# Kernel optimization log

Measured on AMD Instinct MI355X. Metric: run time of the kernel, lower is better.

The kernel has to match this reference:

```python
import jax, jax.numpy as jnp
import numpy as np
from jax import lax

DIM = 128
HEADS = 2
SR = 4
HID = 512  # 4 * DIM
DROPKEY_P = 0.1


def _ln(x, g, b, eps=1e-5):
    m = jnp.mean(x, axis=-1, keepdims=True)
    v = jnp.var(x, axis=-1, keepdims=True)
    return (x - m) / jnp.sqrt(v + eps) * g + b


def _block(x, H, W, params, key):
    (n1g, n1b, qw, kvw, srw, srb, sng, snb, pw, pb,
     n2g, n2b, f1w, f1b, dww, dwb, f2w, f2b) = params
    B, N, C = x.shape
    dh = C // HEADS
    scale = dh ** -0.5
    # --- spatial-reduction attention ---
    h = _ln(x, n1g, n1b)
    q = (h @ qw.T).reshape(B, N, HEADS, dh).transpose(0, 2, 1, 3)  # [B,h,N,dh]
    xi = h.transpose(0, 2, 1).reshape(B, C, H, W)
    xs = lax.conv_general_dilated(xi, srw, (SR, SR), 'VALID',
                                  dimension_numbers=('NCHW', 'OIHW', 'NCHW'))
    xs = xs + srb[None, :, None, None]
    Np = (H // SR) * (W // SR)
    xs = xs.reshape(B, C, Np).transpose(0, 2, 1)  # [B,N',C]
    xs = _ln(xs, sng, snb)
    kv = (xs @ kvw.T).reshape(B, Np, 2, HEADS, dh).transpose(2, 0, 3, 1, 4)
    k, v = kv[0], kv[1]  # [B,h,N',dh]
    attn = jnp.einsum('bhnd,bhmd->bhnm', q, k) * scale
    # dropkey: bernoulli(p) mask pushed to -1e12 before softmax (always applied)
    mask = jax.random.bernoulli(key, DROPKEY_P, attn.shape)
    attn = attn + mask.astype(attn.dtype) * (-1e12)
    attn = jax.nn.softmax(attn, axis=-1)
    o = jnp.einsum('bhnm,bhmd->bhnd', attn, v).transpose(0, 2, 1, 3).reshape(B, N, C)
    x = x + o @ pw.T + pb
    # --- MLP with depthwise conv ---
    h2 = _ln(x, n2g, n2b)
    h2 = h2 @ f1w.T + f1b  # [B,N,HID]
    hi = h2.transpose(0, 2, 1).reshape(B, HID, H, W)
    hi = lax.conv_general_dilated(hi, dww, (1, 1), 'SAME',
                                  feature_group_count=HID,
                                  dimension_numbers=('NCHW', 'OIHW', 'NCHW'))
    hi = hi + dwb[None, :, None, None]
    h2 = hi.reshape(B, HID, N).transpose(0, 2, 1)
    h2 = jax.nn.gelu(h2, approximate=False)
    x = x + h2 @ f2w.T + f2b
    return x


def setup_inputs() -> dict:
    key = jax.random.key(0)
    ks = jax.random.split(key, 10)
    p = {}
    p['x'] = jax.random.normal(ks[0], (16, 2 * DIM, 56, 56), jnp.float32)
    p['concat_w'] = jax.random.normal(ks[1], (DIM, 2 * DIM), jnp.float32) * 0.02
    p['concat_b'] = jnp.zeros((DIM,), jnp.float32)
    # two Blocks -> leading dim 2 on all per-block params
    p['norm1_g'] = jnp.ones((2, DIM), jnp.float32)
    p['norm1_b'] = jnp.zeros((2, DIM), jnp.float32)
    p['q_w'] = jax.random.normal(ks[2], (2, DIM, DIM), jnp.float32) * 0.02
    p['kv_w'] = jax.random.normal(ks[3], (2, 2 * DIM, DIM), jnp.float32) * 0.02
    p['sr_w'] = jax.random.normal(ks[4], (2, DIM, DIM, SR, SR), jnp.float32) * 0.03
    p['sr_b'] = jnp.zeros((2, DIM), jnp.float32)
    p['srn_g'] = jnp.ones((2, DIM), jnp.float32)
    p['srn_b'] = jnp.zeros((2, DIM), jnp.float32)
    p['proj_w'] = jax.random.normal(ks[5], (2, DIM, DIM), jnp.float32) * 0.02
    p['proj_b'] = jnp.zeros((2, DIM), jnp.float32)
    p['norm2_g'] = jnp.ones((2, DIM), jnp.float32)
    p['norm2_b'] = jnp.zeros((2, DIM), jnp.float32)
    p['fc1_w'] = jax.random.normal(ks[6], (2, HID, DIM), jnp.float32) * 0.02
    p['fc1_b'] = jnp.zeros((2, HID), jnp.float32)
    p['dw_w'] = jax.random.normal(ks[7], (2, HID, 1, 3, 3), jnp.float32) * 0.1
    p['dw_b'] = jnp.zeros((2, HID), jnp.float32)
    p['fc2_w'] = jax.random.normal(ks[8], (2, DIM, HID), jnp.float32) * 0.02
    p['fc2_b'] = jnp.zeros((2, DIM), jnp.float32)
    return p


def reference(x, concat_w, concat_b, norm1_g, norm1_b, q_w, kv_w, sr_w, sr_b,
              srn_g, srn_b, proj_w, proj_b, norm2_g, norm2_b, fc1_w, fc1_b,
              dw_w, dw_b, fc2_w, fc2_b):
    b, c, h, w = x.shape
    xs = x.transpose(0, 2, 3, 1).reshape(b, h * w, c)
    xs = xs @ concat_w.T + concat_b  # [B,N,DIM]
    mkey = jax.random.key(42)
    stacked = (norm1_g, norm1_b, q_w, kv_w, sr_w, sr_b, srn_g, srn_b, proj_w,
               proj_b, norm2_g, norm2_b, fc1_w, fc1_b, dw_w, dw_b, fc2_w, fc2_b)
    for i in range(2):
        params_i = tuple(p[i] for p in stacked)
        xs = _block(xs, h, w, params_i, jax.random.fold_in(mkey, i))
    return xs.reshape(b, h, w, DIM).transpose(0, 3, 1, 2)
```

## Files before the change

kernel.cpp:

```cpp
#include <hip/hip_runtime.h>
#include <stdint.h>

typedef __attribute__((ext_vector_type(8))) short short8;
typedef __attribute__((ext_vector_type(4))) float f32x4;
typedef __attribute__((ext_vector_type(2))) float f32x2;
typedef unsigned short u16;
typedef uint32_t u32;
typedef unsigned long long u64;

__host__ __device__ static inline void threefry(u32 k0, u32 k1, u32 x0, u32 x1,
                                                u32* o0, u32* o1) {
  u32 ks2 = k0 ^ k1 ^ 0x1BD11BDAu;
  x0 += k0; x1 += k1;
#define TF_RR(r) { x0 += x1; x1 = (x1 << (r)) | (x1 >> (32 - (r))); x1 ^= x0; }
  TF_RR(13) TF_RR(15) TF_RR(26) TF_RR(6)
  x0 += k1;  x1 += ks2 + 1u;
  TF_RR(17) TF_RR(29) TF_RR(16) TF_RR(24)
  x0 += ks2; x1 += k0 + 2u;
  TF_RR(13) TF_RR(15) TF_RR(26) TF_RR(6)
  x0 += k0;  x1 += k1 + 3u;
  TF_RR(17) TF_RR(29) TF_RR(16) TF_RR(24)
  x0 += k1;  x1 += ks2 + 4u;
  TF_RR(13) TF_RR(15) TF_RR(26) TF_RR(6)
  x0 += ks2; x1 += k0 + 5u;
#undef TF_RR
  *o0 = x0; *o1 = x1;
}

__device__ static inline float bf2f(u16 u) {
  union { u32 i; float f; } v; v.i = ((u32)u) << 16; return v.f;
}
__device__ static inline u16 f2bf(float f) {
  union { float f; u32 i; } v; v.f = f;
  u32 x = v.i;
  return (u16)((x + 0x7FFFu + ((x >> 16) & 1u)) >> 16);
}
__device__ static inline float lo_bf(u32 w) {
  union { u32 i; float f; } v; v.i = w << 16; return v.f;
}
__device__ static inline float hi_bf(u32 w) {
  union { u32 i; float f; } v; v.i = w & 0xFFFF0000u; return v.f;
}
__device__ static inline bool is_f32(const u32* ng) { return ng[0] == 0x3F800000u; }

typedef const uint32_t __attribute__((address_space(1)))* gas_ptr;
typedef uint32_t __attribute__((address_space(3)))* las_ptr;
__device__ static inline void gld16(const u16* g, u16* l) {
  __builtin_amdgcn_global_load_lds((gas_ptr)(const void*)g, (las_ptr)(void*)l, 16, 0, 0);
}

#define MASK_HALF 9834496u
#define MASK_HALFWORDS 307328

__global__ __launch_bounds__(256) void mask_gen(u32* __restrict__ Mw, u32 k0, u32 k1) {
  int w = blockIdx.x * 256 + threadIdx.x;
  if (w >= MASK_HALFWORDS) return;
  u32 bits0 = 0, bits1 = 0;
  u32 base = (u32)w * 32u;
  for (int i = 0; i < 32; i++) {
    u32 o0, o1;
    threefry(k0, k1, base + (u32)i, base + (u32)i + MASK_HALF, &o0, &o1);
    union { u32 u; float f; } u0, u1;
    u0.u = (o0 >> 9) | 0x3F800000u;
    u1.u = (o1 >> 9) | 0x3F800000u;
    if (u0.f - 1.0f < 0.1f) bits0 |= (1u << i);
    if (u1.f - 1.0f < 0.1f) bits1 |= (1u << i);
  }
  Mw[w] = bits0;
  Mw[w + MASK_HALFWORDS] = bits1;
}

__global__ __launch_bounds__(256) void mask_repack(const u32* __restrict__ MSK,
                                                   u32* __restrict__ MSK2) {
  int t = blockIdx.x * 256 + threadIdx.x;
  if (t >= 702464) return;
  int row = t / 7, w = t - row * 7;
  u32 f0 = (u32)row * 196u + (u32)w * 32u;
  u32 lo = MSK[f0 >> 5], hi = MSK[(f0 >> 5) + 1];
  int sh = f0 & 31;
  MSK2[t] = sh ? ((lo >> sh) | (hi << (32 - sh))) : lo;
}

__global__ __launch_bounds__(256) void zero_vt(u32* __restrict__ VT) {
  int t = blockIdx.x * 256 + threadIdx.x;
  if (t < 229376) VT[t] = 0;
}

struct PtrTab { const void* p[20]; };
#define ARENA_N 963968

__global__ __launch_bounds__(256) void convert_params(PtrTab tab, u16* __restrict__ arena) {
  const int cum[21] = {0, 32768, 32896, 33152, 33408, 66176, 131712, 656000, 656256,
                       656512, 656768, 689536, 689792, 690048, 690304, 821376, 822400,
                       831616, 832640, 963712, 963968};
  int idx = blockIdx.x * 256 + threadIdx.x;
  if (idx >= ARENA_N) return;
  bool f32m = (((const u32*)tab.p[2])[0] == 0x3F800000u);
  int t = 0;
  while (idx >= cum[t + 1]) t++;
  int local = idx - cum[t];
  if (t == 16) {
    int blk = local / 4608, r = local - blk * 4608;
    int wi = r >> 9, c = r & 511;
    local = blk * 4608 + c * 9 + wi;
  }
  u16 v;
  if (f32m) v = f2bf(((const float*)tab.p[t])[local]);
  else      v = ((const u16*)tab.p[t])[local];
  arena[idx] = v;
}

__global__ __launch_bounds__(256) void transpose_in(const void* __restrict__ Xin,
                                                    const u32* __restrict__ ng,
                                                    u16* __restrict__ Xt) {
  bool f32m = is_f32(ng);
  __shared__ u16 tile[64][65];
  int n0 = blockIdx.x * 64, c0 = blockIdx.y * 64, b = blockIdx.z;
  int tx = threadIdx.x & 63, ty = threadIdx.x >> 6;
  if (f32m) {
    const float* src = (const float*)Xin + (size_t)b * 256 * 3136;
#pragma unroll
    for (int i = 0; i < 16; i++) {
      int cl = i * 4 + ty;
      tile[cl][tx] = f2bf(src[(size_t)(c0 + cl) * 3136 + n0 + tx]);
    }
  } else {
    const u16* src = (const u16*)Xin + (size_t)b * 256 * 3136;
#pragma unroll
    for (int i = 0; i < 16; i++) {
      int cl = i * 4 + ty;
      tile[cl][tx] = src[(size_t)(c0 + cl) * 3136 + n0 + tx];
    }
  }
  __syncthreads();
  u16* dst = Xt + (size_t)b * 3136 * 256;
#pragma unroll
  for (int i = 0; i < 16; i++) {
    int nl = i * 4 + ty;
    dst[(size_t)(n0 + nl) * 256 + c0 + tx] = tile[tx][nl];
  }
}

__global__ __launch_bounds__(256) void transpose_out(const float* __restrict__ X,
                                                     const u32* __restrict__ ng,
                                                     void* __restrict__ Out) {
  bool f32m = is_f32(ng);
  __shared__ float tile[64][65];
  int n0 = blockIdx.x * 64, d0 = blockIdx.y * 64, b = blockIdx.z;
  int tx = threadIdx.x & 63, ty = threadIdx.x >> 6;
#pragma unroll
  for (int i = 0; i < 16; i++) {
    int nl = i * 4 + ty;
    tile[nl][tx] = X[((size_t)b * 3136 + n0 + nl) * 128 + d0 + tx];
  }
  __syncthreads();
#pragma unroll
  for (int i = 0; i < 16; i++) {
    int dl = i * 4 + ty;
    size_t o = ((size_t)b * 128 + d0 + dl) * 3136 + n0 + tx;
    if (f32m) ((float*)Out)[o] = tile[tx][dl];
    else      ((u16*)Out)[o]   = f2bf(tile[tx][dl]);
  }
}

__global__ __launch_bounds__(256) void ln_kernel(const float* __restrict__ X,
                                                 const u16* __restrict__ G,
                                                 const u16* __restrict__ Bi,
                                                 u16* __restrict__ Out, int rows) {
  int row = blockIdx.x * 4 + (threadIdx.x >> 6);
  if (row >= rows) return;
  int lane = threadIdx.x & 63;
  const float* xp = X + (size_t)row * 128;
  float a = xp[lane], c = xp[lane + 64];
  float s1 = a + c, s2 = a * a + c * c;
#pragma unroll
  for (int d = 1; d < 64; d <<= 1) {
    s1 += __shfl_xor(s1, d);
    s2 += __shfl_xor(s2, d);
  }
  float mean = s1 * 0.0078125f;
  float var = s2 * 0.0078125f - mean * mean;
  float inv = 1.0f / sqrtf(var + 1e-5f);
  Out[(size_t)row * 128 + lane] = f2bf((a - mean) * inv * bf2f(G[lane]) + bf2f(Bi[lane]));
  Out[(size_t)row * 128 + lane + 64] =
      f2bf((c - mean) * inv * bf2f(G[lane + 64]) + bf2f(Bi[lane + 64]));
}

__global__ __launch_bounds__(256) void im2col_sr(const u16* __restrict__ H,
                                                 u16* __restrict__ Acol) {
  int t = blockIdx.x * 256 + threadIdx.x;
  int c = t & 127;
  int rest = t >> 7;
  int ij = rest & 15;
  int row = rest >> 4;
  int i = ij >> 2, j = ij & 3;
  int bb = row / 196, pp = row - bb * 196;
  int ph = pp / 14, pw = pp - ph * 14;
  int n = (4 * ph + i) * 56 + 4 * pw + j;
  Acol[(size_t)row * 2048 + c * 16 + ij] = H[((size_t)bb * 3136 + n) * 128 + c];
}

__global__ __launch_bounds__(256) __attribute__((amdgpu_waves_per_eu(2, 4)))
void gemm_tiled(const u16* __restrict__ A,
                const u16* __restrict__ W,
                const u16* __restrict__ bias,
                float* __restrict__ outF,
                u16* __restrict__ outB,
                u16* __restrict__ outVT,
                int M, int N, int K, int mode) {
  __shared__ __align__(16) u16 smem[16896];
  u16* AlsP = smem;
  u16* BlsP = smem + 8192;
  int n0 = blockIdx.x * 128, m0 = blockIdx.y * 128;
  int tid = threadIdx.x, wv = tid >> 6, lane = tid & 63;
  int wr = wv >> 1, wc = wv & 1;
  int l15 = lane & 15, hh = lane >> 4, lk = hh * 8;
  int srow = wv * 32 + (lane >> 2);
  int scol = (lane & 3) * 8;

  f32x4 acc[4][4];
#pragma unroll
  for (int m = 0; m < 4; m++)
#pragma unroll
    for (int n = 0; n < 4; n++) acc[m][n] = (f32x4){0.f, 0.f, 0.f, 0.f};

#define STAGE(buf, k0)                                                          \
  {                                                                             \
    _Pragma("unroll") for (int i = 0; i < 2; i++) {                             \
      int ar = m0 + srow + i * 16;                                              \
      if (ar >= M) ar = M - 1;                                                  \
      gld16(A + (size_t)ar * K + (k0) + scol,                                   \
            AlsP + (buf) * 4096 + (wv * 32 + i * 16) * 32);                     \
      int br = n0 + srow + i * 16;                                              \
      gld16(W + (size_t)br * K + (k0) + scol,                                   \
            BlsP + (buf) * 4096 + (wv * 32 + i * 16) * 32);                     \
    }                                                                           \
  }

  int nt = K >> 5;
  STAGE(0, 0);
  int cur = 0;
  for (int t = 0; t < nt; t++) {
    __syncthreads();
    if (t + 1 < nt) STAGE(cur ^ 1, (t + 1) * 32);
    short8 af[4], bf[4];
#pragma unroll
    for (int m = 0; m < 4; m++)
      af[m] = *(const short8*)(AlsP + cur * 4096 + (wr * 64 + m * 16 + l15) * 32 + lk);
#pragma unroll
    for (int n = 0; n < 4; n++)
      bf[n] = *(const short8*)(BlsP + cur * 4096 + (wc * 64 + n * 16 + l15) * 32 + lk);
#pragma unroll
    for (int m = 0; m < 4; m++)
#pragma unroll
      for (int n = 0; n < 4; n++)
        acc[m][n] = __builtin_amdgcn_mfma_f32_16x16x32_bf16(af[m], bf[n], acc[m][n], 0, 0, 0);
    cur ^= 1;
  }
#undef STAGE

  if (mode == 0) {
    __syncthreads();
#pragma unroll
    for (int n = 0; n < 4; n++) {
      int col = wc * 64 + n * 16 + l15;
      float bv = bias ? bf2f(bias[n0 + col]) : 0.0f;
#pragma unroll
      for (int m = 0; m < 4; m++) {
        int rbase = wr * 64 + m * 16 + hh * 4;
#pragma unroll
        for (int r = 0; r < 4; r++)
          smem[(rbase + r) * 132 + col] = f2bf(acc[m][n][r] + bv);
      }
    }
    __syncthreads();
#pragma unroll
    for (int p = 0; p < 8; p++) {
      int row = p * 16 + (tid >> 4);
      int colb = (tid & 15) * 8;
      int grow = m0 + row;
      if (grow < M) {
        short8 v = *(const short8*)&smem[row * 132 + colb];
        *(short8*)(outB + (size_t)grow * N + n0 + colb) = v;
      }
    }
    return;
  }

#pragma unroll
  for (int n = 0; n < 4; n++) {
    int col = n0 + wc * 64 + n * 16 + l15;
    float bv = bias ? bf2f(bias[col]) : 0.0f;
#pragma unroll
    for (int m = 0; m < 4; m++) {
      int rbase = m0 + wr * 64 + m * 16 + hh * 4;
#pragma unroll
      for (int r = 0; r < 4; r++) {
        int row = rbase + r;
        if (row < M) {
          float v = acc[m][n][r] + bv;
          if (mode == 1) outF[(size_t)row * N + col] = v;
          else if (mode == 2) outF[(size_t)row * N + col] += v;
          else {
            if (col < 128) outB[(size_t)row * 128 + col] = f2bf(v);
            else {
              int hd = (col - 128) >> 6, d = (col - 128) & 63;
              int b = row / 196, key = row - b * 196;
              outVT[(size_t)((b * 2 + hd) * 64 + d) * 224 + key] = f2bf(v);
            }
          }
        }
      }
    }
  }
}

__global__ __launch_bounds__(256) __attribute__((amdgpu_waves_per_eu(2, 4)))
void gemm_n128(const u16* __restrict__ A,
               const u16* __restrict__ W,
               const u16* __restrict__ bias,
               float* __restrict__ outF,
               u16* __restrict__ outB,
               const u16* __restrict__ lnG,
               const u16* __restrict__ lnB,
               u16* __restrict__ outH,
               int M, int K, int mode) {
  __shared__ __align__(16) u16 smem[12288];
  __shared__ float sumsA[64][4];
  __shared__ float sumsB[64][4];
  u16* Als = smem;
  u16* Bls = smem + 4096;
  int m0 = blockIdx.y * 64;
  int tid = threadIdx.x, wv = tid >> 6, lane = tid & 63;
  int l15 = lane & 15, hq = lane >> 4, lk = hq * 8;
  int scol = (lane & 3) * 8;

  f32x4 acc[4][2];
#pragma unroll
  for (int m = 0; m < 4; m++)
#pragma unroll
    for (int n = 0; n < 2; n++) acc[m][n] = (f32x4){0.f, 0.f, 0.f, 0.f};

#define STAGE(buf, k0)                                                          \
  {                                                                             \
    int ar = m0 + wv * 16 + (lane >> 2);                                        \
    if (ar >= M) ar = M - 1;                                                    \
    gld16(A + (size_t)ar * K + (k0) + scol, Als + (buf) * 2048 + wv * 512);     \
    _Pragma("unroll") for (int i = 0; i < 2; i++) {                             \
      int br = wv * 32 + i * 16 + (lane >> 2);                                  \
      gld16(W + (size_t)br * K + (k0) + scol,                                   \
            Bls + (buf) * 4096 + wv * 1024 + i * 512);                          \
    }                                                                           \
  }

  int nt = K >> 5;
  STAGE(0, 0);
  int cur = 0;
  for (int t = 0; t < nt; t++) {
    __syncthreads();
    if (t + 1 < nt) STAGE(cur ^ 1, (t + 1) * 32);
    short8 af[4], bf[2];
#pragma unroll
    for (int m = 0; m < 4; m++)
      af[m] = *(const short8*)(Als + cur * 2048 + (m * 16 + l15) * 32 + lk);
#pragma unroll
    for (int n = 0; n < 2; n++)
      bf[n] = *(const short8*)(Bls + cur * 4096 + (wv * 32 + n * 16 + l15) * 32 + lk);
#pragma unroll
    for (int m = 0; m < 4; m++)
#pragma unroll
      for (int n = 0; n < 2; n++)
        acc[m][n] = __builtin_amdgcn_mfma_f32_16x16x32_bf16(af[m], bf[n], acc[m][n], 0, 0, 0);
    cur ^= 1;
  }
#undef STAGE

  if (mode == 2) {
#pragma unroll
    for (int n = 0; n < 2; n++) {
      int col = wv * 32 + n * 16 + l15;
      float bv = bias ? bf2f(bias[col]) : 0.0f;
#pragma unroll
      for (int m = 0; m < 4; m++) {
        int rbase = m0 + m * 16 + hq * 4;
#pragma unroll
        for (int r = 0; r < 4; r++)
          outF[(size_t)(rbase + r) * 128 + col] += acc[m][n][r] + bv;
      }
    }
    return;
  }

  if (mode >= 4) {
#pragma unroll
    for (int n = 0; n < 2; n++) {
      int col = wv * 32 + n * 16 + l15;
      float bv = bias ? bf2f(bias[col]) : 0.0f;
#pragma unroll
      for (int m = 0; m < 4; m++) {
        int rbase = m0 + m * 16 + hq * 4;
#pragma unroll
        for (int r = 0; r < 4; r++) {
          float v = acc[m][n][r] + bv;
          if (mode == 5) v += outF[(size_t)(rbase + r) * 128 + col];
          acc[m][n][r] = v;
          outF[(size_t)(rbase + r) * 128 + col] = v;
        }
      }
    }
#pragma unroll
    for (int m = 0; m < 4; m++) {
#pragma unroll
      for (int r = 0; r < 4; r++) {
        float a = acc[m][0][r] + acc[m][1][r];
        float b = acc[m][0][r] * acc[m][0][r] + acc[m][1][r] * acc[m][1][r];
#pragma unroll
        for (int d = 1; d < 16; d <<= 1) {
          a += __shfl_xor(a, d);
          b += __shfl_xor(b, d);
        }
        if (l15 == 0) {
          int lrow = m * 16 + hq * 4 + r;
          sumsA[lrow][wv] = a;
          sumsB[lrow][wv] = b;
        }
      }
    }
    __syncthreads();
#pragma unroll
    for (int m = 0; m < 4; m++) {
#pragma unroll
      for (int r = 0; r < 4; r++) {
        int lrow = m * 16 + hq * 4 + r;
        float t1 = sumsA[lrow][0] + sumsA[lrow][1] + sumsA[lrow][2] + sumsA[lrow][3];
        float t2 = sumsB[lrow][0] + sumsB[lrow][1] + sumsB[lrow][2] + sumsB[lrow][3];
        float mean = t1 * 0.0078125f;
        float var = t2 * 0.0078125f - mean * mean;
        float inv = 1.0f / sqrtf(var + 1e-5f);
#pragma unroll
        for (int n = 0; n < 2; n++) {
          int col = wv * 32 + n * 16 + l15;
          float g = bf2f(lnG[col]), bb2 = bf2f(lnB[col]);
          smem[lrow * 132 + col] = f2bf((acc[m][n][r] - mean) * inv * g + bb2);
        }
      }
    }
    __syncthreads();
#pragma unroll
    for (int p = 0; p < 4; p++) {
      int row = p * 16 + (tid >> 4);
      int colb = (tid & 15) * 8;
      short8 v = *(const short8*)&smem[row * 132 + colb];
      *(short8*)(outH + (size_t)(m0 + row) * 128 + colb) = v;
    }
    return;
  }

  __syncthreads();
#pragma unroll
  for (int n = 0; n < 2; n++) {
    int col = wv * 32 + n * 16 + l15;
    float bv = bias ? bf2f(bias[col]) : 0.0f;
#pragma unroll
    for (int m = 0; m < 4; m++) {
      int rbase = m * 16 + hq * 4;
#pragma unroll
      for (int r = 0; r < 4; r++)
        smem[(rbase + r) * 132 + col] = f2bf(acc[m][n][r] + bv);
    }
  }
  __syncthreads();
#pragma unroll
  for (int p = 0; p < 4; p++) {
    int row = p * 16 + (tid >> 4);
    int colb = (tid & 15) * 8;
    short8 v = *(const short8*)&smem[row * 132 + colb];
    *(short8*)(outB + (size_t)(m0 + row) * 128 + colb) = v;
  }
}

__global__ __launch_bounds__(256) void gemm_splitk(const u16* __restrict__ A,
                                                   const u16* __restrict__ W,
                                                   float* __restrict__ PS,
                                                   int M, int N, int K) {
  __shared__ __align__(16) u16 Als[2][4096];
  __shared__ __align__(16) u16 Bls[2][4096];
  int n0 = blockIdx.x * 128, m0 = blockIdx.y * 128, ks = blockIdx.z;
  int tid = threadIdx.x, wv = tid >> 6, lane = tid & 63;
  int wr = wv >> 1, wc = wv & 1;
  int l15 = lane & 15, lk = (lane >> 4) * 8;
  int srow = wv * 32 + (lane >> 2);
  int scol = (lane & 3) * 8;

  f32x4 acc[4][4];
#pragma unroll
  for (int m = 0; m < 4; m++)
#pragma unroll
    for (int n = 0; n < 4; n++) acc[m][n] = (f32x4){0.f, 0.f, 0.f, 0.f};

#define STAGE(buf, k0)                                                          \
  {                                                                             \
    _Pragma("unroll") for (int i = 0; i < 2; i++) {                             \
      int ar = m0 + srow + i * 16;                                              \
      if (ar >= M) ar = M - 1;                                                  \
      gld16(A + (size_t)ar * K + (k0) + scol,                                   \
            &Als[buf][(wv * 32 + i * 16) * 32]);                                \
      int br = n0 + srow + i * 16;                                              \
      gld16(W + (size_t)br * K + (k0) + scol,                                   \
            &Bls[buf][(wv * 32 + i * 16) * 32]);                                \
    }                                                                           \
  }

  int kbeg = ks * 128;
  STAGE(0, kbeg);
  int cur = 0;
  for (int t = 0; t < 4; t++) {
    __syncthreads();
    if (t + 1 < 4) STAGE(cur ^ 1, kbeg + (t + 1) * 32);
    short8 af[4], bf[4];
#pragma unroll
    for (int m = 0; m < 4; m++)
      af[m] = *(const short8*)(&Als[cur][(wr * 64 + m * 16 + l15) * 32 + lk]);
#pragma unroll
    for (int n = 0; n < 4; n++)
      bf[n] = *(const short8*)(&Bls[cur][(wc * 64 + n * 16 + l15) * 32 + lk]);
#pragma unroll
    for (int m = 0; m < 4; m++)
#pragma unroll
      for (int n = 0; n < 4; n++)
        acc[m][n] = __builtin_amdgcn_mfma_f32_16x16x32_bf16(af[m], bf[n], acc[m][n], 0, 0, 0);
    cur ^= 1;
  }
#undef STAGE

  float* myPS = PS + (size_t)ks * M * N;
#pragma unroll
  for (int n = 0; n < 4; n++) {
    int col = n0 + wc * 64 + n * 16 + l15;
#pragma unroll
    for (int m = 0; m < 4; m++) {
      int rbase = m0 + wr * 64 + m * 16 + (lane >> 4) * 4;
#pragma unroll
      for (int r = 0; r < 4; r++) {
        int row = rbase + r;
        if (row < M) myPS[(size_t)row * N + col] = acc[m][n][r];
      }
    }
  }
}

__global__ __launch_bounds__(256) void splitk_reduce(const float* __restrict__ PS,
                                                     const u16* __restrict__ bias,
                                                     float* __restrict__ XS) {
  int t = blockIdx.x * 256 + threadIdx.x;
  if (t >= 401408) return;
  float s = bf2f(bias[t & 127]);
#pragma unroll
  for (int k = 0; k < 16; k++) s += PS[(size_t)k * 401408 + t];
  XS[t] = s;
}

__global__ __launch_bounds__(256) __attribute__((amdgpu_waves_per_eu(2, 4)))
void attn_kernel(const u16* __restrict__ Q,
                 const u16* __restrict__ Kb,
                 const u16* __restrict__ VT,
                 const u32* __restrict__ M2,
                 u16* __restrict__ O) {
  __shared__ __align__(16) u16 smA[14848];
  int t = blockIdx.x;
  int tp = (t & 7) * 196 + (t >> 3);
  int bh = tp / 49, qt = tp - bh * 49;
  int b = bh >> 1, hd = bh & 1;
  int q0 = qt * 64;
  int tid = threadIdx.x;

  int wv = tid >> 6, lane = tid & 63;
  int l15 = lane & 15, h = lane >> 4, lk = h * 8;

  {
    const u16* ksrc = Kb + (size_t)b * 196 * 128 + hd * 64;
    for (int idx = tid; idx < 1568; idx += 256) {
      int row = idx >> 3, ch = idx & 7;
      short8 v = *(const short8*)(ksrc + (size_t)row * 128 + ch * 8);
      *(short8*)&smA[row * 68 + ch * 8] = v;
    }
  }

  const u16* qp = Q + ((size_t)(b * 3136 + q0 + wv * 16 + l15) * 128) + hd * 64 + lk;
  short8 aq0 = *(const short8*)(qp);
  short8 aq1 = *(const short8*)(qp + 32);
  int rowg = q0 + wv * 16 + h * 4;

  u32 mwv[4][7];
  const u32* mwbase = M2 + (size_t)(bh * 3136 + rowg) * 7;
#pragma unroll
  for (int r = 0; r < 4; r++)
#pragma unroll
    for (int w = 0; w < 7; w++) mwv[r][w] = mwbase[r * 7 + w];

  __syncthreads();

  float sarr[13][4];
#pragma unroll
  for (int cc = 0; cc < 13; cc++) {
    int key = cc * 16 + l15;
    int keyc = key > 195 ? 195 : key;
    short8 kb0 = *(const short8*)&smA[keyc * 68 + lk];
    short8 kb1 = *(const short8*)&smA[keyc * 68 + 32 + lk];
    f32x4 s = {0.f, 0.f, 0.f, 0.f};
    s = __builtin_amdgcn_mfma_f32_16x16x32_bf16(aq0, kb0, s, 0, 0, 0);
    s = __builtin_amdgcn_mfma_f32_16x16x32_bf16(aq1, kb1, s, 0, 0, 0);
#pragma unroll
    for (int r = 0; r < 4; r++) sarr[cc][r] = s[r] * 0.125f;
  }

#pragma unroll
  for (int cc = 0; cc < 13; cc++) {
    bool keyok = (cc * 16 + l15) < 196;
    int pos = (cc & 3) * 16 + l15;
#pragma unroll
    for (int r = 0; r < 4; r++) {
      u64 mm = (cc < 4) ? ((u64)mwv[r][0] | ((u64)mwv[r][1] << 32))
             : (cc < 8) ? ((u64)mwv[r][2] | ((u64)mwv[r][3] << 32))
             : (cc < 12) ? ((u64)mwv[r][4] | ((u64)mwv[r][5] << 32))
                         : ((u64)mwv[r][6]);
      bool drop = (mm >> pos) & 1ull;
      if (!keyok || drop) sarr[cc][r] = -3.0e38f;
    }
  }

  float mx[4] = {sarr[0][0], sarr[0][1], sarr[0][2], sarr[0][3]};
#pragma unroll
  for (int cc = 1; cc < 13; cc++)
#pragma unroll
    for (int r = 0; r < 4; r++) mx[r] = fmaxf(mx[r], sarr[cc][r]);
#pragma unroll
  for (int d = 1; d < 16; d <<= 1)
#pragma unroll
    for (int r = 0; r < 4; r++) mx[r] = fmaxf(mx[r], __shfl_xor(mx[r], d));
  float sm[4] = {0.f, 0.f, 0.f, 0.f};
#pragma unroll
  for (int cc = 0; cc < 13; cc++)
#pragma unroll
    for (int r = 0; r < 4; r++) {
      float p = __expf(sarr[cc][r] - mx[r]);
      sarr[cc][r] = p;
      sm[r] += p;
    }
#pragma unroll
  for (int d = 1; d < 16; d <<= 1)
#pragma unroll
    for (int r = 0; r < 4; r++) sm[r] += __shfl_xor(sm[r], d);
  float inv[4];
#pragma unroll
  for (int r = 0; r < 4; r++)
    asm("v_rcp_f32 %0, %1" : "=v"(inv[r]) : "v"(sm[r]));

  __syncthreads();

#pragma unroll
  for (int cc = 0; cc < 13; cc++)
#pragma unroll
    for (int r = 0; r < 4; r++)
      smA[(wv * 16 + h * 4 + r) * 232 + cc * 16 + l15] = f2bf(sarr[cc][r] * inv[r]);
#pragma unroll
  for (int rj = 0; rj < 4; rj++) smA[(wv * 16 + l15) * 232 + 208 + h * 4 + rj] = 0;

  const u16* vbase = VT + (size_t)(bh * 64) * 224;
  short8 vw[4];
#pragma unroll
  for (int i = 0; i < 4; i++) {
    vw[i] = *(const short8*)(vbase + (size_t)(0 * 16 + l15) * 224 + i * 32 + lk);
  }
#pragma unroll
  for (int dc = 0; dc < 4; dc++) {
    f32x4 oa = {0.f, 0.f, 0.f, 0.f};
#pragma unroll
    for (int kc = 0; kc < 7; kc++) {
      int i = dc * 7 + kc;
      short8 bv = vw[i & 3];
      if (i + 4 < 28) {
        int i2 = i + 4;
        int dc2 = i2 / 7, kc2 = i2 - dc2 * 7;
        vw[i & 3] =
            *(const short8*)(vbase + (size_t)(dc2 * 16 + l15) * 224 + kc2 * 32 + lk);
      }
      short8 a = *(const short8*)&smA[(wv * 16 + l15) * 232 + kc * 32 + lk];
      oa = __builtin_amdgcn_mfma_f32_16x16x32_bf16(a, bv, oa, 0, 0, 0);
    }
#pragma unroll
    for (int r = 0; r < 4; r++) {
      O[((size_t)(b * 3136 + rowg + r) * 128) + hd * 64 + dc * 16 + l15] = f2bf(oa[r]);
    }
  }
}

__global__ __launch_bounds__(256) __attribute__((amdgpu_waves_per_eu(2, 4)))
void dwconv_gelu(const u16* __restrict__ H2,
                 const u16* __restrict__ Wdw,
                 const u16* __restrict__ Bdw,
                 u16* __restrict__ Out) {
  int tid = threadIdx.x;
  int wv = tid >> 6, lane = tid & 63;
  int sb = blockIdx.x;
  int wg = (sb & 7) * 392 + (sb >> 3);
  int strip = wg * 4 + wv;
  int bb = strip / 784;
  int s = strip - bb * 784;
  int y = s / 14, x0 = (s - y * 14) * 4;
  int c0 = lane * 8;

  f32x2 wf[9][4];
#pragma unroll
  for (int t9 = 0; t9 < 9; t9++) {
    short8 w8 = *(const short8*)(Wdw + t9 * 512 + c0);
#pragma unroll
    for (int p = 0; p < 4; p++) {
      u32 w = ((const u32*)&w8)[p];
      wf[t9][p] = (f32x2){lo_bf(w), hi_bf(w)};
    }
  }
  f32x2 acc[4][4];
  {
    short8 b8 = *(const short8*)(Bdw + c0);
#pragma unroll
    for (int p = 0; p < 4; p++) {
      u32 w = ((const u32*)&b8)[p];
      f32x2 bv = {lo_bf(w), hi_bf(w)};
#pragma unroll
      for (int q = 0; q < 4; q++) acc[q][p] = bv;
    }
  }

  const u16* base = H2 + ((size_t)bb * 3136) * 512 + c0;
#pragma unroll
  for (int di = -1; di <= 1; di++) {
    int y2 = y + di;
    if (y2 < 0 || y2 >= 56) continue;
    const u16* rowp = base + (size_t)(y2 * 56) * 512;
#pragma unroll
    for (int j = 0; j < 6; j++) {
      int c = x0 - 1 + j;
      if (c < 0 || c > 55) continue;
      short8 h8 = *(const short8*)(rowp + (size_t)c * 512);
      f32x2 hf[4];
#pragma unroll
      for (int p = 0; p < 4; p++) {
        u32 w = ((const u32*)&h8)[p];
        hf[p] = (f32x2){lo_bf(w), hi_bf(w)};
      }
      int wrow = (di + 1) * 3;
#pragma unroll
      for (int q = 0; q < 4; q++) {
        int dx = j - 1 - q;
        if (dx < -1 || dx > 1) continue;
#pragma unroll
        for (int p = 0; p < 4; p++) acc[q][p] += hf[p] * wf[wrow + dx + 1][p];
      }
    }
  }

  size_t obase = ((size_t)(bb * 3136 + y * 56 + x0)) * 512 + c0;
#pragma unroll
  for (int q = 0; q < 4; q++) {
    short8 ov;
#pragma unroll
    for (int p = 0; p < 4; p++) {
      float g2[2];
#pragma unroll
      for (int e = 0; e < 2; e++) {
        float v = acc[q][p][e];
        float tt = v * v;
        float yn = v * (-2.3022088f - 0.1029434f * tt);
        float ex;
        asm("v_exp_f32 %0, %1" : "=v"(ex) : "v"(yn));
        float den = 1.0f + ex;
        float sg;
        asm("v_rcp_f32 %0, %1" : "=v"(sg) : "v"(den));
        g2[e] = v * sg;
      }
      u32 pk;
      asm("v_cvt_pk_bf16_f32 %0, %1, %2" : "=v"(pk) : "v"(g2[0]), "v"(g2[1]));
      ((u32*)&ov)[p] = pk;
    }
    *(short8*)(Out + obase + (size_t)q * 512) = ov;
  }
}

__global__ __launch_bounds__(256) void fill_sentinel(void* __restrict__ Out,
                                                     const u32* __restrict__ ng, int n) {
  bool f32m = is_f32(ng);
  int t = blockIdx.x * 256 + threadIdx.x;
  if (t >= n) return;
  if (f32m) ((float*)Out)[t] = 12345.0f;
  else      ((u16*)Out)[t]   = f2bf(12345.0f);
}

extern "C" void kernel_launch(void* const* d_in, const int* in_sizes, int n_in,
                              void* d_out, int out_size, void* d_ws, size_t ws_size,
                              hipStream_t stream) {
  (void)in_sizes; (void)n_in;
  const u32* ng = (const u32*)d_in[3];

  const size_t o_X   = 0;
  const size_t o_H   = 25690112;
  const size_t o_R   = o_H + 12845056;
  const size_t o_Q   = o_R;
  const size_t o_O   = o_R + 12845056;
  const size_t o_Xt  = o_R + 25690112;
  const size_t o_H2C = o_R;
  const size_t o_H2  = o_R + 51380224;
  const size_t o_XS  = o_H2 + 51380224;
  const size_t o_XSN = o_XS + 1605632;
  const size_t o_KB  = o_XSN + 802816;
  const size_t o_VT  = o_KB + 802816;
  const size_t o_M2  = o_VT + 917504;
  const size_t o_AR  = o_M2 + 2809856;
  const size_t NEED  = o_AR + (size_t)ARENA_N * 2;

  if (ws_size < NEED) {
    fill_sentinel<<<(out_size + 255) / 256, 256, 0, stream>>>(d_out, ng, out_size);
    return;
  }

  char* ws = (char*)d_ws;
  float* X  = (float*)(ws + o_X);
  u16* H    = (u16*)(ws + o_H);
  u16* Qb   = (u16*)(ws + o_Q);
  u16* Ob   = (u16*)(ws + o_O);
  u16* Xt   = (u16*)(ws + o_Xt);
  u16* H2C  = (u16*)(ws + o_H2C);
  u16* H2   = (u16*)(ws + o_H2);
  float* PS = (float*)(ws + o_H2);
  float* XS = (float*)(ws + o_XS);
  u16* XSN  = (u16*)(ws + o_XSN);
  u16* Kb   = (u16*)(ws + o_KB);
  u16* VT   = (u16*)(ws + o_VT);
  u32* MSK  = (u32*)(ws + o_Xt);
  u32* MSK2 = (u32*)(ws + o_M2);
  u16* AR   = (u16*)(ws + o_AR);

  PtrTab tab;
  for (int j = 0; j < 20; j++) tab.p[j] = d_in[j + 1];
  convert_params<<<(ARENA_N + 255) / 256, 256, 0, stream>>>(tab, AR);
  zero_vt<<<896, 256, 0, stream>>>((u32*)VT);

  u16* ACW  = AR + 0;      u16* ACB  = AR + 32768;
  u16* AN1G = AR + 32896;  u16* AN1B = AR + 33152;
  u16* AQW  = AR + 33408;  u16* AKVW = AR + 66176;
  u16* ASRW = AR + 131712; u16* ASRB = AR + 656000;
  u16* ASNG = AR + 656256; u16* ASNB = AR + 656512;
  u16* APW  = AR + 656768; u16* APB  = AR + 689536;
  u16* AN2G = AR + 689792; u16* AN2B = AR + 690048;
  u16* AF1W = AR + 690304; u16* AF1B = AR + 821376;
  u16* ADWW = AR + 822400; u16* ADWB = AR + 831616;
  u16* AF2W = AR + 832640; u16* AF2B = AR + 963712;

  transpose_in<<<dim3(49, 4, 16), 256, 0, stream>>>(d_in[0], ng, Xt);
  gemm_n128<<<dim3(1, 784), 256, 0, stream>>>(Xt, ACW, ACB, X, nullptr,
                                              AN1G, AN1B, H, 50176, 256, 4);

  for (int i = 0; i < 2; i++) {
    u32 fk0, fk1;
    threefry(0u, 42u, 0u, (u32)i, &fk0, &fk1);

    gemm_n128<<<dim3(1, 784), 256, 0, stream>>>(H, AQW + i * 16384, nullptr, nullptr,
                                                Qb, nullptr, nullptr, nullptr,
                                                50176, 128, 0);
    im2col_sr<<<25088, 256, 0, stream>>>(H, Xt);
    gemm_splitk<<<dim3(1, 25, 16), 256, 0, stream>>>(Xt, ASRW + i * 262144, PS,
                                                     3136, 128, 2048);
    splitk_reduce<<<1568, 256, 0, stream>>>(PS, ASRB + i * 128, XS);
    mask_gen<<<1201, 256, 0, stream>>>(MSK, fk0, fk1);
    mask_repack<<<2744, 256, 0, stream>>>(MSK, MSK2);

    ln_kernel<<<784, 256, 0, stream>>>(XS, ASNG + i * 128, ASNB + i * 128, XSN, 3136);
    gemm_tiled<<<dim3(2, 25), 256, 0, stream>>>(XSN, AKVW + i * 32768, nullptr, nullptr,
                                                Kb, VT, 3136, 256, 128, 3);
    attn_kernel<<<1568, 256, 0, stream>>>(Qb, Kb, VT, MSK2, Ob);
    gemm_n128<<<dim3(1, 784), 256, 0, stream>>>(Ob, APW + i * 16384, APB + i * 128,
                                                X, nullptr,
                                                AN2G + i * 128, AN2B + i * 128, H,
                                                50176, 128, 5);
    gemm_tiled<<<dim3(4, 392), 256, 0, stream>>>(H, AF1W + i * 65536, AF1B + i * 512,
                                                 nullptr, H2, nullptr,
                                                 50176, 512, 128, 0);
    dwconv_gelu<<<3136, 256, 0, stream>>>(H2, ADWW + i * 4608, ADWB + i * 512, H2C);
    if (i == 0) {
      gemm_n128<<<dim3(1, 784), 256, 0, stream>>>(H2C, AF2W, AF2B, X, nullptr,
                                                  AN1G + 128, AN1B + 128, H,
                                                  50176, 512, 5);
    } else {
      gemm_n128<<<dim3(1, 784), 256, 0, stream>>>(H2C, AF2W + 65536, AF2B + 128,
                                                  X, nullptr, nullptr, nullptr, nullptr,
                                                  50176, 512, 2);
    }
  }

  transpose_out<<<dim3(49, 2, 16), 256, 0, stream>>>(X, ng, d_out);
}
```

Baseline: 490.8 us.

## Fuse small kernels: mask gen+repack, splitk reduce+LN, zero into convert; stage V in LDS

Merges mask generation and repacking into one kernel that writes the row-aligned mask layout directly. Fuses the split-K reduction with the following LayerNorm, and folds VT zeroing into the parameter conversion launch, removing several launches and an intermediate fp32 buffer. In attention, V tiles are now staged in shared memory instead of being prefetched from global memory into registers. The extra LDS buffer raises shared memory per block and may reduce occupancy.

```diff
diff --git a/kernel.cpp b/kernel.cpp
--- a/kernel.cpp
+++ b/kernel.cpp
@@ -50,51 +50,44 @@
 }
 
 #define MASK_HALF 9834496u
-#define MASK_HALFWORDS 307328
-
-__global__ __launch_bounds__(256) void mask_gen(u32* __restrict__ Mw, u32 k0, u32 k1) {
-  int w = blockIdx.x * 256 + threadIdx.x;
-  if (w >= MASK_HALFWORDS) return;
+
+__global__ __launch_bounds__(256) void mask_gen2(u32* __restrict__ MSK2, u32 k0, u32 k1) {
+  int t = blockIdx.x * 256 + threadIdx.x;
+  if (t >= 351232) return;
+  int w = t % 7;
+  int rowbh = t / 7;
+  u32 base = (u32)rowbh * 196u + (u32)w * 32u;
+  int kmax = 196 - w * 32;
+  if (kmax > 32) kmax = 32;
   u32 bits0 = 0, bits1 = 0;
-  u32 base = (u32)w * 32u;
-  for (int i = 0; i < 32; i++) {
+  for (int j = 0; j < kmax; j++) {
     u32 o0, o1;
-    threefry(k0, k1, base + (u32)i, base + (u32)i + MASK_HALF, &o0, &o1);
+    threefry(k0, k1, base + (u32)j, base + (u32)j + MASK_HALF, &o0, &o1);
     union { u32 u; float f; } u0, u1;
     u0.u = (o0 >> 9) | 0x3F800000u;
     u1.u = (o1 >> 9) | 0x3F800000u;
-    if (u0.f - 1.0f < 0.1f) bits0 |= (1u << i);
-    if (u1.f - 1.0f < 0.1f) bits1 |= (1u << i);
-  }
-  Mw[w] = bits0;
-  Mw[w + MASK_HALFWORDS] = bits1;
-}
-
-__global__ __launch_bounds__(256) void mask_repack(const u32* __restrict__ MSK,
-                                                   u32* __restrict__ MSK2) {
-  int t = blockIdx.x * 256 + threadIdx.x;
-  if (t >= 702464) return;
-  int row = t / 7, w = t - row * 7;
-  u32 f0 = (u32)row * 196u + (u32)w * 32u;
-  u32 lo = MSK[f0 >> 5], hi = MSK[(f0 >> 5) + 1];
-  int sh = f0 & 31;
-  MSK2[t] = sh ? ((lo >> sh) | (hi << (32 - sh))) : lo;
-}
-
-__global__ __launch_bounds__(256) void zero_vt(u32* __restrict__ VT) {
-  int t = blockIdx.x * 256 + threadIdx.x;
-  if (t < 229376) VT[t] = 0;
+    if (u0.f - 1.0f < 0.1f) bits0 |= (1u << j);
+    if (u1.f - 1.0f < 0.1f) bits1 |= (1u << j);
+  }
+  MSK2[(size_t)rowbh * 7 + w] = bits0;
+  MSK2[(size_t)(rowbh + 50176) * 7 + w] = bits1;
 }
 
 struct PtrTab { const void* p[20]; };
 #define ARENA_N 963968
-
-__global__ __launch_bounds__(256) void convert_params(PtrTab tab, u16* __restrict__ arena) {
+#define VT_WORDS 229376
+
+__global__ __launch_bounds__(256) void convert_params(PtrTab tab, u16* __restrict__ arena,
+                                                      u32* __restrict__ VT) {
   const int cum[21] = {0, 32768, 32896, 33152, 33408, 66176, 131712, 656000, 656256,
                        656512, 656768, 689536, 689792, 690048, 690304, 821376, 822400,
                        831616, 832640, 963712, 963968};
   int idx = blockIdx.x * 256 + threadIdx.x;
-  if (idx >= ARENA_N) return;
+  if (idx >= ARENA_N) {
+    int v = idx - ARENA_N;
+    if (v < VT_WORDS) VT[v] = 0;
+    return;
+  }
   bool f32m = (((const u32*)tab.p[2])[0] == 0x3F800000u);
   int t = 0;
   while (idx >= cum[t + 1]) t++;
@@ -161,29 +154,6 @@
     if (f32m) ((float*)Out)[o] = tile[tx][dl];
     else      ((u16*)Out)[o]   = f2bf(tile[tx][dl]);
   }
-}
-
-__global__ __launch_bounds__(256) void ln_kernel(const float* __restrict__ X,
-                                                 const u16* __restrict__ G,
-                                                 const u16* __restrict__ Bi,
-                                                 u16* __restrict__ Out, int rows) {
-  int row = blockIdx.x * 4 + (threadIdx.x >> 6);
-  if (row >= rows) return;
-  int lane = threadIdx.x & 63;
-  const float* xp = X + (size_t)row * 128;
-  float a = xp[lane], c = xp[lane + 64];
-  float s1 = a + c, s2 = a * a + c * c;
-#pragma unroll
-  for (int d = 1; d < 64; d <<= 1) {
-    s1 += __shfl_xor(s1, d);
-    s2 += __shfl_xor(s2, d);
-  }
-  float mean = s1 * 0.0078125f;
-  float var = s2 * 0.0078125f - mean * mean;
-  float inv = 1.0f / sqrtf(var + 1e-5f);
-  Out[(size_t)row * 128 + lane] = f2bf((a - mean) * inv * bf2f(G[lane]) + bf2f(Bi[lane]));
-  Out[(size_t)row * 128 + lane + 64] =
-      f2bf((c - mean) * inv * bf2f(G[lane + 64]) + bf2f(Bi[lane + 64]));
 }
 
 __global__ __launch_bounds__(256) void im2col_sr(const u16* __restrict__ H,
@@ -549,15 +519,35 @@
   }
 }
 
-__global__ __launch_bounds__(256) void splitk_reduce(const float* __restrict__ PS,
-                                                     const u16* __restrict__ bias,
-                                                     float* __restrict__ XS) {
-  int t = blockIdx.x * 256 + threadIdx.x;
-  if (t >= 401408) return;
-  float s = bf2f(bias[t & 127]);
+__global__ __launch_bounds__(256) void splitk_reduce_ln(const float* __restrict__ PS,
+                                                        const u16* __restrict__ bias,
+                                                        const u16* __restrict__ G,
+                                                        const u16* __restrict__ Bi,
+                                                        u16* __restrict__ XSN) {
+  __shared__ float red[4][2];
+  int tid = threadIdx.x;
+  int row = blockIdx.x * 2 + (tid >> 7);
+  int col = tid & 127;
+  int t = row * 128 + col;
+  float s = bf2f(bias[col]);
 #pragma unroll
   for (int k = 0; k < 16; k++) s += PS[(size_t)k * 401408 + t];
-  XS[t] = s;
+  float s1 = s, s2 = s * s;
+#pragma unroll
+  for (int d = 1; d < 64; d <<= 1) {
+    s1 += __shfl_xor(s1, d);
+    s2 += __shfl_xor(s2, d);
+  }
+  int wv = tid >> 6;
+  if ((tid & 63) == 0) { red[wv][0] = s1; red[wv][1] = s2; }
+  __syncthreads();
+  int other = wv ^ 1;
+  float t1 = red[wv][0] + red[other][0];
+  float t2 = red[wv][1] + red[other][1];
+  float mean = t1 * 0.0078125f;
+  float var = t2 * 0.0078125f - mean * mean;
+  float inv = 1.0f / sqrtf(var + 1e-5f);
+  XSN[t] = f2bf((s - mean) * inv * bf2f(G[col]) + bf2f(Bi[col]));
 }
 
 __global__ __launch_bounds__(256) __attribute__((amdgpu_waves_per_eu(2, 4)))
@@ -567,6 +557,7 @@
                  const u32* __restrict__ M2,
                  u16* __restrict__ O) {
   __shared__ __align__(16) u16 smA[14848];
+  __shared__ __align__(16) u16 smV[14848];
   int t = blockIdx.x;
   int tp = (t & 7) * 196 + (t >> 3);
   int bh = tp / 49, qt = tp - bh * 49;
@@ -583,6 +574,13 @@
       int row = idx >> 3, ch = idx & 7;
       short8 v = *(const short8*)(ksrc + (size_t)row * 128 + ch * 8);
       *(short8*)&smA[row * 68 + ch * 8] = v;
+    }
+    const u16* vsrc = VT + (size_t)(bh * 64) * 224;
+    for (int idx = tid; idx < 64 * 29; idx += 256) {
+      int d = idx / 29, c8 = idx - d * 29;
+      short8 v = {0, 0, 0, 0, 0, 0, 0, 0};
+      if (c8 < 28) v = *(const short8*)(vsrc + (size_t)d * 224 + c8 * 8);
+      *(short8*)&smV[d * 232 + c8 * 8] = v;
     }
   }
 
@@ -666,26 +664,13 @@
 #pragma unroll
   for (int rj = 0; rj < 4; rj++) smA[(wv * 16 + l15) * 232 + 208 + h * 4 + rj] = 0;
 
-  const u16* vbase = VT + (size_t)(bh * 64) * 224;
-  short8 vw[4];
-#pragma unroll
-  for (int i = 0; i < 4; i++) {
-    vw[i] = *(const short8*)(vbase + (size_t)(0 * 16 + l15) * 224 + i * 32 + lk);
-  }
 #pragma unroll
   for (int dc = 0; dc < 4; dc++) {
     f32x4 oa = {0.f, 0.f, 0.f, 0.f};
 #pragma unroll
     for (int kc = 0; kc < 7; kc++) {
-      int i = dc * 7 + kc;
-      short8 bv = vw[i & 3];
-      if (i + 4 < 28) {
-        int i2 = i + 4;
-        int dc2 = i2 / 7, kc2 = i2 - dc2 * 7;
-        vw[i & 3] =
-            *(const short8*)(vbase + (size_t)(dc2 * 16 + l15) * 224 + kc2 * 32 + lk);
-      }
       short8 a = *(const short8*)&smA[(wv * 16 + l15) * 232 + kc * 32 + lk];
+      short8 bv = *(const short8*)&smV[(dc * 16 + l15) * 232 + kc * 32 + lk];
       oa = __builtin_amdgcn_mfma_f32_16x16x32_bf16(a, bv, oa, 0, 0, 0);
     }
 #pragma unroll
@@ -810,8 +795,7 @@
   const size_t o_Xt  = o_R + 25690112;
   const size_t o_H2C = o_R;
   const size_t o_H2  = o_R + 51380224;
-  const size_t o_XS  = o_H2 + 51380224;
-  const size_t o_XSN = o_XS + 1605632;
+  const size_t o_XSN = o_H2 + 51380224;
   const size_t o_KB  = o_XSN + 802816;
   const size_t o_VT  = o_KB + 802816;
   const size_t o_M2  = o_VT + 917504;
@@ -832,18 +816,15 @@
   u16* H2C  = (u16*)(ws + o_H2C);
   u16* H2   = (u16*)(ws + o_H2);
   float* PS = (float*)(ws + o_H2);
-  float* XS = (float*)(ws + o_XS);
   u16* XSN  = (u16*)(ws + o_XSN);
   u16* Kb   = (u16*)(ws + o_KB);
   u16* VT   = (u16*)(ws + o_VT);
-  u32* MSK  = (u32*)(ws + o_Xt);
   u32* MSK2 = (u32*)(ws + o_M2);
   u16* AR   = (u16*)(ws + o_AR);
 
   PtrTab tab;
   for (int j = 0; j < 20; j++) tab.p[j] = d_in[j + 1];
-  convert_params<<<(ARENA_N + 255) / 256, 256, 0, stream>>>(tab, AR);
-  zero_vt<<<896, 256, 0, stream>>>((u32*)VT);
+  convert_params<<<(ARENA_N + VT_WORDS + 255) / 256, 256, 0, stream>>>(tab, AR, (u32*)VT);
 
   u16* ACW  = AR + 0;      u16* ACB  = AR + 32768;
   u16* AN1G = AR + 32896;  u16* AN1B = AR + 33152;
@@ -870,11 +851,10 @@
     im2col_sr<<<25088, 256, 0, stream>>>(H, Xt);
     gemm_splitk<<<dim3(1, 25, 16), 256, 0, stream>>>(Xt, ASRW + i * 262144, PS,
                                                      3136, 128, 2048);
-    splitk_reduce<<<1568, 256, 0, stream>>>(PS, ASRB + i * 128, XS);
-    mask_gen<<<1201, 256, 0, stream>>>(MSK, fk0, fk1);
-    mask_repack<<<2744, 256, 0, stream>>>(MSK, MSK2);
-
-    ln_kernel<<<784, 256, 0, stream>>>(XS, ASNG + i * 128, ASNB + i * 128, XSN, 3136);
+    mask_gen2<<<1372, 256, 0, stream>>>(MSK2, fk0, fk1);
+    splitk_reduce_ln<<<1568, 256, 0, stream>>>(PS, ASRB + i * 128,
+                                               ASNG + i * 128, ASNB + i * 128, XSN);
+
     gemm_tiled<<<dim3(2, 25), 256, 0, stream>>>(XSN, AKVW + i * 32768, nullptr, nullptr,
                                                 Kb, VT, 3136, 256, 128, 3);
     attn_kernel<<<1568, 256, 0, stream>>>(Qb, Kb, VT, MSK2, Ob);
```

Result: no change. 497.7 us (+1.4%).
